# Kernel optimization log

Hardware: AMD Instinct MI355X
Metric: run time of the kernel (lower is better)

## Reference

```python
import jax, jax.numpy as jnp
import numpy as np

B, N, D, E, L = 8, 4096, 256, 65536, 1  # graphs, padded nodes, d_model, padded edges, num_layers


def setup_inputs() -> dict:
    key = jax.random.key(0)
    ks = jax.random.split(key, 9)
    x = jax.random.normal(ks[0], (B, N, D), dtype=jnp.float32)
    edge_index = jax.random.randint(ks[1], (B, 2, E), 0, N)
    edge_weight = jax.random.uniform(ks[2], (B, E), dtype=jnp.float32)
    mask = jax.random.randint(ks[3], (B, N), 0, 2).astype(jnp.int32)
    s = 1.0 / np.sqrt(D)
    # GatedGraphConv per-layer linear weight [L, D, D]
    W = jax.random.uniform(ks[4], (L, D, D), jnp.float32, -s, s)
    # GRUCell parameters (r, z, n stacked)
    W_ih = jax.random.uniform(ks[5], (3 * D, D), jnp.float32, -s, s)
    W_hh = jax.random.uniform(ks[6], (3 * D, D), jnp.float32, -s, s)
    b_ih = jax.random.uniform(ks[7], (3 * D,), jnp.float32, -s, s)
    b_hh = jax.random.uniform(ks[8], (3 * D,), jnp.float32, -s, s)
    return {"x": x, "edge_index": edge_index, "edge_weight": edge_weight,
            "mask": mask, "W": W, "W_ih": W_ih, "W_hh": W_hh,
            "b_ih": b_ih, "b_hh": b_hh}


def _gated_graph_conv(x, u, v, ew, W, W_ih, W_hh, b_ih, b_hh):
    """x:[B,N,D]; u,v:[B,E] src/dst indices; ew:[B,E] (already masked)."""
    h = x
    for l in range(L):
        m = jnp.einsum('bnd,de->bne', h, W[l])            # linear transform
        msg = jnp.take_along_axis(m, u[..., None], axis=1) * ew[..., None]  # [B,E,D]
        agg = jax.vmap(lambda ms, vi: jax.ops.segment_sum(ms, vi, num_segments=N))(msg, v)
        # GRUCell(input=agg, hidden=h)
        gi = agg @ W_ih.T + b_ih                          # [B,N,3D]
        gh = h @ W_hh.T + b_hh
        r = jax.nn.sigmoid(gi[..., :D] + gh[..., :D])
        z = jax.nn.sigmoid(gi[..., D:2 * D] + gh[..., D:2 * D])
        n = jnp.tanh(gi[..., 2 * D:] + r * gh[..., 2 * D:])
        h = (1.0 - z) * n + z * h
    return h


def reference(x, edge_index, edge_weight, mask, W, W_ih, W_hh, b_ih, b_hh):
    node_valid = mask > 0                                  # [B,N]
    u = edge_index[:, 0]                                   # source
    v = edge_index[:, 1]                                   # target
    # Drop edges touching invalid nodes: weight -> 0 (equivalent under sum aggr)
    e_valid = jnp.take_along_axis(node_valid, u, axis=1) & jnp.take_along_axis(node_valid, v, axis=1)
    ew = edge_weight * e_valid.astype(edge_weight.dtype)
    h = _gated_graph_conv(x, u, v, ew, W, W_ih, W_hh, b_ih, b_hh)
    # Invalid nodes stay zero (original writes only valid rows of a zeros output)
    return h * node_valid[..., None].astype(h.dtype)
```

## Files before the change

kernel.cpp:

```cpp
#include <hip/hip_runtime.h>
#include <math.h>

#define Bn 8
#define Nn 4096
#define Dn 256
#define En 65536

typedef __bf16 bf8 __attribute__((ext_vector_type(8)));
typedef float f4 __attribute__((ext_vector_type(4)));
typedef unsigned short us8 __attribute__((ext_vector_type(8)));

__device__ __forceinline__ float4 ld4(const float* p) { return *(const float4*)p; }

__device__ __forceinline__ unsigned short f2bf(float f) {
    union { float f; unsigned int u; } v; v.f = f;
    unsigned int r = v.u + 0x7fff + ((v.u >> 16) & 1);
    return (unsigned short)(r >> 16);
}
__device__ __forceinline__ float bf2f(unsigned short h) {
    union { unsigned int u; float f; } v; v.u = (unsigned int)h << 16;
    return v.f;
}


__device__ __forceinline__ void stage16c(const unsigned short* __restrict__ gchunk,
                                         int stride, char* ldschunk, int lane) {
    int u = lane >> 3, s = lane & 7;
    int xx = s ^ (u & 7);
    const unsigned short* g = gchunk + (size_t)(2 * u + (xx >> 2)) * stride + (xx & 3) * 8;
    __builtin_amdgcn_global_load_lds((const __attribute__((address_space(1))) void*)g,
                                     (__attribute__((address_space(3))) void*)ldschunk,
                                     16, 0, 0);
}

__device__ __forceinline__ bf8 fragld(const unsigned short* region, int r, int q) {
    int s = (((r & 1) << 2) | q) ^ ((r >> 1) & 7);
    return *(const bf8*)(region + (r >> 1) * 64 + s * 8);
}

__device__ __forceinline__ void ldswrite8(unsigned short* region, int r, int q,
                                          const unsigned short* vals) {
    int s = (((r & 1) << 2) | q) ^ ((r >> 1) & 7);
    *(us8*)(region + (r >> 1) * 64 + s * 8) = *(const us8*)vals;
}


__device__ void rowscan_piece(const int* __restrict__ mask, int* __restrict__ rowidx,
                              int* __restrict__ rowcnt, int* part) {
    int t = threadIdx.x;
    int base = t * 128;
    unsigned long long b0 = 0, b1 = 0;
    int s = 0;
#pragma unroll 8
    for (int i = 0; i < 64; i++) {
        int m = mask[base + i] > 0;
        b0 |= (unsigned long long)m << i; s += m;
    }
#pragma unroll 8
    for (int i = 0; i < 64; i++) {
        int m = mask[base + 64 + i] > 0;
        b1 |= (unsigned long long)m << i; s += m;
    }
    part[t] = s;
    __syncthreads();
    for (int st = 1; st < 256; st <<= 1) {
        int v = (t >= st) ? part[t - st] : 0;
        __syncthreads();
        part[t] += v;
        __syncthreads();
    }
    int run = part[t] - s;
    for (int i = 0; i < 64; i++)
        if ((b0 >> i) & 1) rowidx[run++] = base + i;
    for (int i = 0; i < 64; i++)
        if ((b1 >> i) & 1) rowidx[run++] = base + 64 + i;
    if (t == 255) rowcnt[0] = part[255];
}

__device__ void wf_piece(int wfi, const float* __restrict__ Wih, const float* __restrict__ W,
                         unsigned short* __restrict__ Ball, unsigned short* lds) {
    int t = threadIdx.x, lane = t & 63, w = t >> 6;
    int wr = w >> 1, wc = w & 1, q = lane >> 4, c16 = lane & 15;
    int o0 = (wfi % 6) * 128, d0b = (wfi / 6) * 64;
    f4 acc[4][2];
    f4 zz = {0.f, 0.f, 0.f, 0.f};
#pragma unroll
    for (int rt = 0; rt < 4; rt++)
#pragma unroll
        for (int ct = 0; ct < 2; ct++) acc[rt][ct] = zz;

    int r = t >> 1, half = t & 1;
    for (int k0 = 0; k0 < 256; k0 += 32) {
        const float* pa = Wih + (size_t)(o0 + r) * 256 + k0 + half * 16;
        float4 a0 = ld4(pa), a1 = ld4(pa + 4), a2 = ld4(pa + 8), a3 = ld4(pa + 12);
        float4 b0, b1, b2, b3;
        if (t < 128) {
            const float* pb = W + (size_t)(d0b + r) * 256 + k0 + half * 16;
            b0 = ld4(pb); b1 = ld4(pb + 4); b2 = ld4(pb + 8); b3 = ld4(pb + 12);
        }
        __syncthreads();
        unsigned short tmp[16];
        tmp[0] = f2bf(a0.x); tmp[1] = f2bf(a0.y); tmp[2] = f2bf(a0.z); tmp[3] = f2bf(a0.w);
        tmp[4] = f2bf(a1.x); tmp[5] = f2bf(a1.y); tmp[6] = f2bf(a1.z); tmp[7] = f2bf(a1.w);
        tmp[8] = f2bf(a2.x); tmp[9] = f2bf(a2.y); tmp[10] = f2bf(a2.z); tmp[11] = f2bf(a2.w);
        tmp[12] = f2bf(a3.x); tmp[13] = f2bf(a3.y); tmp[14] = f2bf(a3.z); tmp[15] = f2bf(a3.w);
        ldswrite8(lds, r, half * 2, tmp);
        ldswrite8(lds, r, half * 2 + 1, tmp + 8);
        if (t < 128) {
            unsigned short tb[16];
            tb[0] = f2bf(b0.x); tb[1] = f2bf(b0.y); tb[2] = f2bf(b0.z); tb[3] = f2bf(b0.w);
            tb[4] = f2bf(b1.x); tb[5] = f2bf(b1.y); tb[6] = f2bf(b1.z); tb[7] = f2bf(b1.w);
            tb[8] = f2bf(b2.x); tb[9] = f2bf(b2.y); tb[10] = f2bf(b2.z); tb[11] = f2bf(b2.w);
            tb[12] = f2bf(b3.x); tb[13] = f2bf(b3.y); tb[14] = f2bf(b3.z); tb[15] = f2bf(b3.w);
            ldswrite8(lds + 4096, r, half * 2, tb);
            ldswrite8(lds + 4096, r, half * 2 + 1, tb + 8);
        }
        __syncthreads();
        bf8 a[4];
#pragma unroll
        for (int rt = 0; rt < 4; rt++) a[rt] = fragld(lds, wr * 64 + rt * 16 + c16, q);
#pragma unroll
        for (int ct = 0; ct < 2; ct++) {
            bf8 b = fragld(lds + 4096, wc * 32 + ct * 16 + c16, q);
#pragma unroll
            for (int rt = 0; rt < 4; rt++)
                acc[rt][ct] = __builtin_amdgcn_mfma_f32_16x16x32_bf16(a[rt], b, acc[rt][ct], 0, 0, 0);
        }
    }
#pragma unroll
    for (int ct = 0; ct < 2; ct++) {
        int col = d0b + wc * 32 + ct * 16 + c16;
#pragma unroll
        for (int rt = 0; rt < 4; rt++) {
            int ob = o0 + wr * 64 + rt * 16 + q * 4;
#pragma unroll
            for (int i = 0; i < 4; i++)
                Ball[(size_t)(ob + i) * 512 + col] = f2bf(acc[rt][ct][i]);
        }
    }
}

__global__ __launch_bounds__(256) void setup_kernel(const int* __restrict__ ei,
                                                    const int* __restrict__ mask,
                                                    const float* __restrict__ Wih,
                                                    const float* __restrict__ W,
                                                    const float* __restrict__ Whh,
                                                    int* __restrict__ cnt,
                                                    int* __restrict__ rowidx,
                                                    int* __restrict__ rowcnt,
                                                    unsigned short* __restrict__ Ball,
                                                    float* __restrict__ out) {
    __shared__ __align__(16) unsigned short lds[6144];
    int b = blockIdx.x, t = threadIdx.x;
    if (b == 0) {
        rowscan_piece(mask, rowidx, rowcnt, (int*)lds);
        return;
    }
    if (b < 25) {
        wf_piece(b - 1, Wih, W, Ball, lds);
        return;
    }
    if (b < 217) {
        int i = ((b - 25) * 256 + t) * 4;
        float4 wv = ld4(Whh + i);
        int o = i >> 8, d = i & 255;
        ushort4 ov;
        ov.x = f2bf(wv.x); ov.y = f2bf(wv.y); ov.z = f2bf(wv.z); ov.w = f2bf(wv.w);
        *(ushort4*)(Ball + (size_t)o * 512 + 256 + d) = ov;
        return;
    }
    if (b < 2265) {
        int idx = (b - 217) * 256 + t;
        int bb = idx >> 16, e = idx & 65535;
        const int* eb = ei + (size_t)bb * 2 * En;
        int u = eb[e];
        int v = eb[En + e];
        const int* mb = mask + bb * Nn;
        if (mb[u] > 0 && mb[v] > 0) atomicAdd(&cnt[bb * Nn + v], 1);
        return;
    }
    {
        int zb = b - 2265;
        int r = zb * 8 + (t >> 5);
        if (mask[r] > 0) return;
        int col = (t & 31) * 8;
        float4 z = make_float4(0.f, 0.f, 0.f, 0.f);
        *(float4*)(out + (size_t)r * 256 + col) = z;
        *(float4*)(out + (size_t)r * 256 + col + 4) = z;
    }
}


__global__ __launch_bounds__(256) void scan_kernel(const int* __restrict__ cnt,
                                                   int* __restrict__ off,
                                                   int* __restrict__ cursor) {
    int b = blockIdx.x, t = threadIdx.x;
    __shared__ int chunk[256];
    int local[16];
    int s = 0;
    int base = b * Nn + t * 16;
#pragma unroll
    for (int i = 0; i < 16; i++) { local[i] = cnt[base + i]; s += local[i]; }
    chunk[t] = s;
    __syncthreads();
    for (int st = 1; st < 256; st <<= 1) {
        int v = (t >= st) ? chunk[t - st] : 0;
        __syncthreads();
        chunk[t] += v;
        __syncthreads();
    }
    int run = chunk[t] - s;
    int ob = b * (Nn + 1) + t * 16;
#pragma unroll
    for (int i = 0; i < 16; i++) {
        off[ob + i] = run;
        cursor[base + i] = run;
        run += local[i];
    }
    if (t == 255) off[b * (Nn + 1) + Nn] = run;
}

__global__ __launch_bounds__(256) void fill_kernel(const int* __restrict__ ei,
                                                   const int* __restrict__ mask,
                                                   const float* __restrict__ ew,
                                                   int* __restrict__ cursor,
                                                   int* __restrict__ csr_u,
                                                   float* __restrict__ csr_w) {
    int idx = blockIdx.x * 256 + threadIdx.x;
    int b = idx >> 16;
    int e = idx & 65535;
    const int* eb = ei + (size_t)b * 2 * En;
    int u = eb[e];
    int v = eb[En + e];
    const int* mb = mask + b * Nn;
    if (mb[u] > 0 && mb[v] > 0) {
        int pos = atomicAdd(&cursor[b * Nn + v], 1);
        csr_u[(size_t)b * En + pos] = u;
        csr_w[(size_t)b * En + pos] = ew[(size_t)b * En + e];
    }
}


__global__ __launch_bounds__(256) void agg_kernel(const float* __restrict__ x,
                                                  const int* __restrict__ off,
                                                  const int* __restrict__ csr_u,
                                                  const float* __restrict__ csr_w,
                                                  const int* __restrict__ rowidx,
                                                  const int* __restrict__ rowcnt,
                                                  unsigned short* __restrict__ Ac) {
    int wave = threadIdx.x >> 6, lane = threadIdx.x & 63;
    int i = blockIdx.x * 4 + wave;
    if (i >= rowcnt[0]) return;
    int v = rowidx[i];
    int b = v >> 12, n = v & 4095;
    int s = off[b * (Nn + 1) + n];
    int e = off[b * (Nn + 1) + n + 1];
    const int* cu = csr_u + (size_t)b * En;
    const float* cw = csr_w + (size_t)b * En;
    const float* Xb = x + (size_t)b * Nn * 256;
    float a0 = 0.f, a1 = 0.f, a2 = 0.f, a3 = 0.f;
    int j = s;
    for (; j + 4 <= e; j += 4) {
        int u0 = cu[j], u1 = cu[j + 1], u2 = cu[j + 2], u3 = cu[j + 3];
        float w0 = cw[j], w1 = cw[j + 1], w2 = cw[j + 2], w3 = cw[j + 3];
        float4 m0 = ld4(Xb + (size_t)u0 * 256 + lane * 4);
        float4 m1 = ld4(Xb + (size_t)u1 * 256 + lane * 4);
        float4 m2 = ld4(Xb + (size_t)u2 * 256 + lane * 4);
        float4 m3 = ld4(Xb + (size_t)u3 * 256 + lane * 4);
        a0 += w0 * m0.x + w1 * m1.x + w2 * m2.x + w3 * m3.x;
        a1 += w0 * m0.y + w1 * m1.y + w2 * m2.y + w3 * m3.y;
        a2 += w0 * m0.z + w1 * m1.z + w2 * m2.z + w3 * m3.z;
        a3 += w0 * m0.w + w1 * m1.w + w2 * m2.w + w3 * m3.w;
    }
    for (; j < e; j++) {
        int u = cu[j];
        float wv = cw[j];
        float4 mv = ld4(Xb + (size_t)u * 256 + lane * 4);
        a0 += wv * mv.x; a1 += wv * mv.y; a2 += wv * mv.z; a3 += wv * mv.w;
    }
    ushort4 o;
    o.x = f2bf(a0); o.y = f2bf(a1); o.z = f2bf(a2); o.w = f2bf(a3);
    *(ushort4*)(Ac + (size_t)i * 512 + lane * 4) = o;
    float4 xv = ld4(x + (size_t)v * 256 + lane * 4);
    ushort4 xo;
    xo.x = f2bf(xv.x); xo.y = f2bf(xv.y); xo.z = f2bf(xv.z); xo.w = f2bf(xv.w);
    *(ushort4*)(Ac + (size_t)i * 512 + 256 + lane * 4) = xo;
}


#define GRU_KSTEP(ACCM)                                                                \
    {                                                                                  \
        __syncthreads();                                                               \
        _Pragma("unroll") for (int j = 0; j < 8; j++) {                                \
            int c = w * 8 + j;                                                         \
            const unsigned short* src;                                                 \
            if (c < 8) {                                                               \
                int kh = c >> 2, rg = c & 3;                                           \
                src = Ac + (size_t)(row0 + rg * 16) * 512 + k0 + kh * 32;              \
            } else {                                                                   \
                int bc = c - 8;                                                        \
                int kh = bc / 12, rgB = bc - kh * 12;                                  \
                src = Ball + (size_t)((rgB >> 2) * 256 + d0 + (rgB & 3) * 16) * 512    \
                      + k0 + kh * 32;                                                  \
            }                                                                          \
            stage16c(src, 512, (char*)lds + c * 1024, lane);                           \
        }                                                                              \
        __syncthreads();                                                               \
        _Pragma("unroll") for (int kh = 0; kh < 2; kh++) {                             \
            bf8 a[2];                                                                  \
            a[0] = fragld(lds + (kh * 4 + wr * 2) * 512, c16, q);                      \
            a[1] = fragld(lds + (kh * 4 + wr * 2 + 1) * 512, c16, q);                  \
            _Pragma("unroll") for (int ct = 0; ct < 2; ct++) {                         \
                int cg = wc * 2 + ct;                                                  \
                bf8 br = fragld(lds + 4096 + (kh * 12 + cg) * 512, c16, q);            \
                bf8 bz = fragld(lds + 4096 + (kh * 12 + 4 + cg) * 512, c16, q);        \
                bf8 bm = fragld(lds + 4096 + (kh * 12 + 8 + cg) * 512, c16, q);        \
                _Pragma("unroll") for (int rt = 0; rt < 2; rt++) {                     \
                    acc_r[rt][ct] = __builtin_amdgcn_mfma_f32_16x16x32_bf16(           \
                        a[rt], br, acc_r[rt][ct], 0, 0, 0);                            \
                    acc_z[rt][ct] = __builtin_amdgcn_mfma_f32_16x16x32_bf16(           \
                        a[rt], bz, acc_z[rt][ct], 0, 0, 0);                            \
                    ACCM[rt][ct] = __builtin_amdgcn_mfma_f32_16x16x32_bf16(            \
                        a[rt], bm, ACCM[rt][ct], 0, 0, 0);                             \
                }                                                                      \
            }                                                                          \
        }                                                                              \
    }

__global__ __launch_bounds__(256, 4) void gru_kernel(const unsigned short* __restrict__ Ac,
                                                     const unsigned short* __restrict__ Ball,
                                                     const float* __restrict__ bih,
                                                     const float* __restrict__ bhh,
                                                     const int* __restrict__ rowidx,
                                                     const int* __restrict__ rowcnt,
                                                     float* __restrict__ out) {
    __shared__ __align__(16) unsigned short lds[16384];
    const int t = threadIdx.x;
    const int lane = t & 63, w = t >> 6;
    const int wr = w >> 1, wc = w & 1;
    const int q = lane >> 4, c16 = lane & 15;
    const int row0 = blockIdx.x * 64, d0 = blockIdx.y * 64;
    const int cnt = rowcnt[0];
    if (row0 >= cnt) return;

    f4 acc_r[2][2], acc_z[2][2], acc_gn[2][2], acc_hn[2][2];
    f4 zz = {0.f, 0.f, 0.f, 0.f};
#pragma unroll
    for (int rt = 0; rt < 2; rt++)
#pragma unroll
        for (int ct = 0; ct < 2; ct++) {
            acc_r[rt][ct] = zz; acc_z[rt][ct] = zz;
            acc_gn[rt][ct] = zz; acc_hn[rt][ct] = zz;
        }

    for (int k0 = 0; k0 < 256; k0 += 64) GRU_KSTEP(acc_gn)
    for (int k0 = 256; k0 < 512; k0 += 64) GRU_KSTEP(acc_hn)

#pragma unroll
    for (int ct = 0; ct < 2; ct++) {
        int dd = d0 + wc * 32 + ct * 16 + c16;
        float b_r = bih[dd] + bhh[dd];
        float b_z = bih[dd + 256] + bhh[dd + 256];
        float b_gn = bih[dd + 512];
        float b_hn = bhh[dd + 512];
#pragma unroll
        for (int rt = 0; rt < 2; rt++) {
            int rbase = row0 + wr * 32 + rt * 16 + q * 4;
#pragma unroll
            for (int i = 0; i < 4; i++) {
                int rc = rbase + i;
                if (rc < cnt) {
                    float sr = acc_r[rt][ct][i] + b_r;
                    float sz = acc_z[rt][ct][i] + b_z;
                    float gn = acc_gn[rt][ct][i] + b_gn;
                    float hn = acc_hn[rt][ct][i] + b_hn;
                    float rg = 1.f / (1.f + __expf(-sr));
                    float zg = 1.f / (1.f + __expf(-sz));
                    float pre = gn + rg * hn;
                    float e2 = __expf(2.f * pre);
                    float ng = 1.f - 2.f / (e2 + 1.f);
                    float xv = bf2f(Ac[(size_t)rc * 512 + 256 + dd]);
                    float h = (1.f - zg) * ng + zg * xv;
                    int v = rowidx[rc];
                    out[(size_t)v * 256 + dd] = h;
                }
            }
        }
    }
}


extern "C" void kernel_launch(void* const* d_in, const int* in_sizes, int n_in,
                              void* d_out, int out_size, void* d_ws, size_t ws_size,
                              hipStream_t stream) {
    const float* x   = (const float*)d_in[0];
    const int*   ei  = (const int*)d_in[1];
    const float* ew  = (const float*)d_in[2];
    const int*   msk = (const int*)d_in[3];
    const float* W   = (const float*)d_in[4];
    const float* Wih = (const float*)d_in[5];
    const float* Whh = (const float*)d_in[6];
    const float* bih = (const float*)d_in[7];
    const float* bhh = (const float*)d_in[8];
    float* out = (float*)d_out;

    char* p = (char*)d_ws;
    unsigned short* Ac   = (unsigned short*)p; p += (size_t)Bn * Nn * 512 * 2;
    unsigned short* Ball = (unsigned short*)p; p += (size_t)768 * 512 * 2;
    int* cnt    = (int*)p;    p += (size_t)Bn * Nn * sizeof(int);
    int* off    = (int*)p;    p += (size_t)Bn * (Nn + 1) * sizeof(int);
    int* cursor = (int*)p;    p += (size_t)Bn * Nn * sizeof(int);
    int* csr_u  = (int*)p;    p += (size_t)Bn * En * sizeof(int);
    float* csr_w = (float*)p; p += (size_t)Bn * En * sizeof(float);
    int* rowidx = (int*)p;    p += (size_t)Bn * Nn * sizeof(int);
    int* rowcnt = (int*)p;    p += 128;

    hipMemsetAsync(cnt, 0, (size_t)Bn * Nn * sizeof(int), stream);
    setup_kernel<<<6361, 256, 0, stream>>>(ei, msk, Wih, W, Whh, cnt, rowidx, rowcnt,
                                           Ball, out);
    scan_kernel<<<Bn, 256, 0, stream>>>(cnt, off, cursor);
    fill_kernel<<<(Bn * En) / 256, 256, 0, stream>>>(ei, msk, ew, cursor, csr_u, csr_w);
    agg_kernel<<<(Bn * Nn) / 4, 256, 0, stream>>>(x, off, csr_u, csr_w, rowidx, rowcnt, Ac);
    gru_kernel<<<dim3(512, 4), 256, 0, stream>>>(Ac, Ball, bih, bhh, rowidx, rowcnt, out);
}
```

Measured before the change: 182.7 us.

## Double-buffer GRU LDS staging and batch 8 gathers per aggregation step

The GRU GEMM kernel now splits its 16KB shared memory into two 8KB buffers, each holding a 32-wide K slice. It stages the next slice while computing on the current one, with one barrier per step, so global-to-LDS copies overlap MFMA work. The aggregation kernel now processes edges in predicated groups of 8 with all row loads issued before accumulation, raising memory-level parallelism and removing the scalar tail loop. The cost is more barriers at a smaller K granularity, more registers in the gather loop, and wasted loads for padded edges in short rows.

Result: no change. 181.5 us (-0.7%).

```diff
diff --git a/kernel.cpp b/kernel.cpp
--- a/kernel.cpp
+++ b/kernel.cpp
@@ -259,24 +259,24 @@
     const float* cw = csr_w + (size_t)b * En;
     const float* Xb = x + (size_t)b * Nn * 256;
     float a0 = 0.f, a1 = 0.f, a2 = 0.f, a3 = 0.f;
-    int j = s;
-    for (; j + 4 <= e; j += 4) {
-        int u0 = cu[j], u1 = cu[j + 1], u2 = cu[j + 2], u3 = cu[j + 3];
-        float w0 = cw[j], w1 = cw[j + 1], w2 = cw[j + 2], w3 = cw[j + 3];
-        float4 m0 = ld4(Xb + (size_t)u0 * 256 + lane * 4);
-        float4 m1 = ld4(Xb + (size_t)u1 * 256 + lane * 4);
-        float4 m2 = ld4(Xb + (size_t)u2 * 256 + lane * 4);
-        float4 m3 = ld4(Xb + (size_t)u3 * 256 + lane * 4);
-        a0 += w0 * m0.x + w1 * m1.x + w2 * m2.x + w3 * m3.x;
-        a1 += w0 * m0.y + w1 * m1.y + w2 * m2.y + w3 * m3.y;
-        a2 += w0 * m0.z + w1 * m1.z + w2 * m2.z + w3 * m3.z;
-        a3 += w0 * m0.w + w1 * m1.w + w2 * m2.w + w3 * m3.w;
-    }
-    for (; j < e; j++) {
-        int u = cu[j];
-        float wv = cw[j];
-        float4 mv = ld4(Xb + (size_t)u * 256 + lane * 4);
-        a0 += wv * mv.x; a1 += wv * mv.y; a2 += wv * mv.z; a3 += wv * mv.w;
+    for (int j = s; j < e; j += 8) {
+        int u[8]; float wv[8];
+#pragma unroll
+        for (int k = 0; k < 8; k++) {
+            int jj = j + k;
+            bool ok = jj < e;
+            int idx = ok ? jj : s;
+            u[k] = cu[idx];
+            wv[k] = ok ? cw[idx] : 0.f;
+        }
+        float4 m[8];
+#pragma unroll
+        for (int k = 0; k < 8; k++) m[k] = ld4(Xb + (size_t)u[k] * 256 + lane * 4);
+#pragma unroll
+        for (int k = 0; k < 8; k++) {
+            a0 += wv[k] * m[k].x; a1 += wv[k] * m[k].y;
+            a2 += wv[k] * m[k].z; a3 += wv[k] * m[k].w;
+        }
     }
     ushort4 o;
     o.x = f2bf(a0); o.y = f2bf(a1); o.z = f2bf(a2); o.w = f2bf(a3);
@@ -288,43 +288,38 @@
 }
 
 
-#define GRU_KSTEP(ACCM)                                                                \
-    {                                                                                  \
-        __syncthreads();                                                               \
-        _Pragma("unroll") for (int j = 0; j < 8; j++) {                                \
-            int c = w * 8 + j;                                                         \
-            const unsigned short* src;                                                 \
-            if (c < 8) {                                                               \
-                int kh = c >> 2, rg = c & 3;                                           \
-                src = Ac + (size_t)(row0 + rg * 16) * 512 + k0 + kh * 32;              \
-            } else {                                                                   \
-                int bc = c - 8;                                                        \
-                int kh = bc / 12, rgB = bc - kh * 12;                                  \
-                src = Ball + (size_t)((rgB >> 2) * 256 + d0 + (rgB & 3) * 16) * 512    \
-                      + k0 + kh * 32;                                                  \
-            }                                                                          \
-            stage16c(src, 512, (char*)lds + c * 1024, lane);                           \
-        }                                                                              \
-        __syncthreads();                                                               \
-        _Pragma("unroll") for (int kh = 0; kh < 2; kh++) {                             \
-            bf8 a[2];                                                                  \
-            a[0] = fragld(lds + (kh * 4 + wr * 2) * 512, c16, q);                      \
-            a[1] = fragld(lds + (kh * 4 + wr * 2 + 1) * 512, c16, q);                  \
-            _Pragma("unroll") for (int ct = 0; ct < 2; ct++) {                         \
-                int cg = wc * 2 + ct;                                                  \
-                bf8 br = fragld(lds + 4096 + (kh * 12 + cg) * 512, c16, q);            \
-                bf8 bz = fragld(lds + 4096 + (kh * 12 + 4 + cg) * 512, c16, q);        \
-                bf8 bm = fragld(lds + 4096 + (kh * 12 + 8 + cg) * 512, c16, q);        \
-                _Pragma("unroll") for (int rt = 0; rt < 2; rt++) {                     \
-                    acc_r[rt][ct] = __builtin_amdgcn_mfma_f32_16x16x32_bf16(           \
-                        a[rt], br, acc_r[rt][ct], 0, 0, 0);                            \
-                    acc_z[rt][ct] = __builtin_amdgcn_mfma_f32_16x16x32_bf16(           \
-                        a[rt], bz, acc_z[rt][ct], 0, 0, 0);                            \
-                    ACCM[rt][ct] = __builtin_amdgcn_mfma_f32_16x16x32_bf16(            \
-                        a[rt], bm, ACCM[rt][ct], 0, 0, 0);                             \
-                }                                                                      \
-            }                                                                          \
-        }                                                                              \
+#define GRU_STAGE(kk, bufbase)                                                      \
+    {                                                                               \
+        _Pragma("unroll") for (int j = 0; j < 4; j++) {                             \
+            int c = w * 4 + j;                                                      \
+            const unsigned short* src;                                              \
+            if (c < 4) {                                                            \
+                src = Ac + (size_t)(row0 + c * 16) * 512 + (kk) * 32;               \
+            } else {                                                                \
+                int g = (c - 4) >> 2, cg = (c - 4) & 3;                             \
+                src = Ball + (size_t)(g * 256 + d0 + cg * 16) * 512 + (kk) * 32;    \
+            }                                                                       \
+            stage16c(src, 512, (char*)(bufbase) + c * 1024, lane);                  \
+        }                                                                           \
+    }
+
+#define GRU_COMPUTE(bufbase, ACCM)                                                  \
+    {                                                                               \
+        const unsigned short* rb = (bufbase);                                       \
+        bf8 a0 = fragld(rb + (wr * 2) * 512, c16, q);                               \
+        bf8 a1 = fragld(rb + (wr * 2 + 1) * 512, c16, q);                           \
+        _Pragma("unroll") for (int ct = 0; ct < 2; ct++) {                          \
+            int cg = wc * 2 + ct;                                                   \
+            bf8 br = fragld(rb + (4 + cg) * 512, c16, q);                           \
+            bf8 bz = fragld(rb + (8 + cg) * 512, c16, q);                           \
+            bf8 bm = fragld(rb + (12 + cg) * 512, c16, q);                          \
+            acc_r[0][ct] = __builtin_amdgcn_mfma_f32_16x16x32_bf16(a0, br, acc_r[0][ct], 0, 0, 0); \
+            acc_r[1][ct] = __builtin_amdgcn_mfma_f32_16x16x32_bf16(a1, br, acc_r[1][ct], 0, 0, 0); \
+            acc_z[0][ct] = __builtin_amdgcn_mfma_f32_16x16x32_bf16(a0, bz, acc_z[0][ct], 0, 0, 0); \
+            acc_z[1][ct] = __builtin_amdgcn_mfma_f32_16x16x32_bf16(a1, bz, acc_z[1][ct], 0, 0, 0); \
+            ACCM[0][ct] = __builtin_amdgcn_mfma_f32_16x16x32_bf16(a0, bm, ACCM[0][ct], 0, 0, 0);   \
+            ACCM[1][ct] = __builtin_amdgcn_mfma_f32_16x16x32_bf16(a1, bm, ACCM[1][ct], 0, 0, 0);   \
+        }                                                                           \
     }
 
 __global__ __launch_bounds__(256, 4) void gru_kernel(const unsigned short* __restrict__ Ac,
@@ -353,8 +348,22 @@
             acc_gn[rt][ct] = zz; acc_hn[rt][ct] = zz;
         }
 
-    for (int k0 = 0; k0 < 256; k0 += 64) GRU_KSTEP(acc_gn)
-    for (int k0 = 256; k0 < 512; k0 += 64) GRU_KSTEP(acc_hn)
+    unsigned short* buf0 = lds;
+    unsigned short* buf1 = lds + 8192;
+
+    GRU_STAGE(0, buf0)
+#pragma unroll
+    for (int kk = 0; kk < 8; kk++) {
+        __syncthreads();
+        GRU_STAGE(kk + 1, (kk & 1) ? buf0 : buf1)
+        GRU_COMPUTE((kk & 1) ? buf1 : buf0, acc_gn)
+    }
+#pragma unroll
+    for (int kk = 8; kk < 16; kk++) {
+        __syncthreads();
+        if (kk < 15) GRU_STAGE(kk + 1, (kk & 1) ? buf0 : buf1)
+        GRU_COMPUTE((kk & 1) ? buf1 : buf0, acc_hn)
+    }
 
 #pragma unroll
     for (int ct = 0; ct < 2; ct++) {
```
